# Optimization experiments

Hardware: AMD Instinct MI355X
Metric: run time of the kernel (lower is better)

The kernel has to match this reference:

```python
import jax, jax.numpy as jnp
import numpy as np

NU, NI = 4000, 4000
R, M, OUT = 5, 256, 75
SIDE, FDIM = 64, 128


def setup_inputs() -> dict:
    key = jax.random.key(0)
    ks = jax.random.split(key, 12)
    return {
        "adj_matrix": jax.random.randint(ks[0], (NU, NI), 0, 6, dtype=jnp.int32),
        "u_sideFeat": jax.random.normal(ks[1], (NU, FDIM), dtype=jnp.float32),
        "v_sideFeat": jax.random.normal(ks[2], (NI, FDIM), dtype=jnp.float32),
        "msg_W": jax.random.normal(ks[3], (R, M, NU + NI), dtype=jnp.float32) * 0.05,
        "dense_W": jax.random.normal(ks[4], (OUT, M), dtype=jnp.float32) * 0.05,
        "u_W1": jax.random.normal(ks[5], (SIDE, FDIM), dtype=jnp.float32) * 0.05,
        "u_b1": jax.random.normal(ks[6], (SIDE,), dtype=jnp.float32) * 0.05,
        "u_W2": jax.random.normal(ks[7], (OUT, SIDE), dtype=jnp.float32) * 0.05,
        "v_W1": jax.random.normal(ks[8], (SIDE, FDIM), dtype=jnp.float32) * 0.05,
        "v_b1": jax.random.normal(ks[9], (SIDE,), dtype=jnp.float32) * 0.05,
        "v_W2": jax.random.normal(ks[10], (OUT, SIDE), dtype=jnp.float32) * 0.05,
        "isNegative": 0,
    }


def reference(adj_matrix, u_sideFeat, v_sideFeat, msg_W, dense_W,
              u_W1, u_b1, u_W2, v_W1, v_b1, v_W2, isNegative):
    # isNegative=0, dropout=0 -> one-hot matrices are exact identity slices,
    # so msgLayer(sum_j adj_r[i,j]/C * onehot_j) == (adj_r/C) @ W_r[:, cols].T
    nu, ni = adj_matrix.shape
    r_vals = jnp.arange(1, msg_W.shape[0] + 1, dtype=adj_matrix.dtype)
    # rating-split binary adjacencies [R, NU, NI]
    A = (adj_matrix[None, :, :] == r_vals[:, None, None]).astype(jnp.float32)
    Nu = A.sum(axis=(0, 2))            # user degree over all ratings [NU]
    Nv = A.sum(axis=(0, 1))            # item degree [NI]
    C = jnp.sqrt(Nu[:, None] * Nv[None, :])  # symmetric normalization [NU, NI]
    Csafe = jnp.where(C > 0, C, 1.0)
    An = A / Csafe[None, :, :]
    W_users = msg_W[:, :, :nu]         # [R, M, NU]
    W_items = msg_W[:, :, nu:]         # [R, M, NI]
    # accum='sum' over ratings, then relu
    Hu = jax.nn.relu(jnp.einsum('rui,rmi->um', An, W_items))  # [NU, M]
    Hv = jax.nn.relu(jnp.einsum('rui,rmu->im', An, W_users))  # [NI, M]
    Fu = jax.nn.relu(u_sideFeat @ u_W1.T + u_b1)
    Fv = jax.nn.relu(v_sideFeat @ v_W1.T + v_b1)
    U = jax.nn.relu(Hu @ dense_W.T + Fu @ u_W2.T)
    V = jax.nn.relu(Hv @ dense_W.T + Fv @ v_W2.T)
    return (U, V)
```

## Files before the change

kernel.cpp:

```cpp
#include <hip/hip_runtime.h>
#include <hip/hip_bf16.h>
#include <stdint.h>

#define NU 4000
#define NI 4000
#define RR 5
#define MM 256
#define OUTD 75
#define FDIM 128
#define KP 4096
#define KPH 2048
#define HP_STRIDE 1024000

typedef float f32x4 __attribute__((ext_vector_type(4)));
typedef int   i32x4 __attribute__((ext_vector_type(4)));
typedef short bf16x8 __attribute__((ext_vector_type(8)));

static __device__ __forceinline__ short f2b(float x) {
  __hip_bfloat16 h = __float2bfloat16(x);
  return (short)__builtin_bit_cast(unsigned short, h);
}
static __device__ __forceinline__ float b2f(short x) {
  unsigned int u = ((unsigned int)(unsigned short)x) << 16;
  return __builtin_bit_cast(float, u);
}
static __device__ __forceinline__ bf16x8 cvt8(f32x4 a, f32x4 b) {
  bf16x8 r;
  r[0] = f2b(a[0]); r[1] = f2b(a[1]); r[2] = f2b(a[2]); r[3] = f2b(a[3]);
  r[4] = f2b(b[0]); r[5] = f2b(b[1]); r[6] = f2b(b[2]); r[7] = f2b(b[3]);
  return r;
}

__global__ __launch_bounds__(256) void k_trans(const int* __restrict__ adj,
                                               uint8_t* __restrict__ a8p,
                                               uint8_t* __restrict__ a8tp,
                                               int* __restrict__ Nu,
                                               int* __restrict__ Nv) {
  __shared__ int8_t lp[64][68];
  __shared__ int8_t lt[64][68];
  __shared__ int rowc[64];
  __shared__ int colp[4][64];
  const int i0 = blockIdx.x * 64;
  const int u0 = blockIdx.y * 64;
  const int t = threadIdx.x;
  const int w = t >> 6, lane = t & 63;
  int mycol = 0;
  for (int rep = 0; rep < 16; rep++) {
    const int r = rep * 4 + w;
    const int u = u0 + r, i = i0 + lane;
    int a = (u < NU && i < NI) ? adj[(size_t)u * NI + i] : 0;
    const int nz = (a > 0) ? 1 : 0;
    unsigned long long bal = __ballot(nz);
    if (lane == 0) rowc[r] = (int)__popcll(bal);
    mycol += nz;
    lp[r][lane] = (int8_t)a;
    lt[lane][r] = (int8_t)a;
  }
  colp[w][lane] = mycol;
  __syncthreads();
  {
    const int r = t >> 2, c = t & 3;
    const uint32_t* xp = (const uint32_t*)(&lp[r][c * 16]);
    const uint32_t* xt = (const uint32_t*)(&lt[r][c * 16]);
    uint32_t t0, t1, t2, t3, w0, w1;
    t0 = xp[0] | (xp[0] >> 4); t1 = xp[1] | (xp[1] >> 4);
    t2 = xp[2] | (xp[2] >> 4); t3 = xp[3] | (xp[3] >> 4);
    w0 = __builtin_amdgcn_perm(t1, t0, 0x06040200u);
    w1 = __builtin_amdgcn_perm(t3, t2, 0x06040200u);
    *(uint2*)(a8p + (size_t)(u0 + r) * KPH + (i0 >> 1) + c * 8) = make_uint2(w0, w1);
    t0 = xt[0] | (xt[0] >> 4); t1 = xt[1] | (xt[1] >> 4);
    t2 = xt[2] | (xt[2] >> 4); t3 = xt[3] | (xt[3] >> 4);
    w0 = __builtin_amdgcn_perm(t1, t0, 0x06040200u);
    w1 = __builtin_amdgcn_perm(t3, t2, 0x06040200u);
    *(uint2*)(a8tp + (size_t)(i0 + r) * KPH + (u0 >> 1) + c * 8) = make_uint2(w0, w1);
  }
  if (t < 64) {
    const int cc = colp[0][t] + colp[1][t] + colp[2][t] + colp[3][t];
    if (i0 + t < NI && cc) atomicAdd(&Nv[i0 + t], cc);
    if (u0 + t < NU && rowc[t]) atomicAdd(&Nu[u0 + t], rowc[t]);
  }
}

__global__ __launch_bounds__(256) void k_pbuild(const float* __restrict__ msgW,
                                                const int* __restrict__ Nu,
                                                const int* __restrict__ Nv,
                                                int8_t* __restrict__ Pu,
                                                int8_t* __restrict__ Pv) {
  const int b = blockIdx.x;
  const float* src = msgW + (size_t)b * (NU + NI);
#pragma unroll
  for (int it = 0; it < 2; ++it) {
    const int base = (threadIdx.x + it * 256) * 8;
    uint32_t lou = 0, hiu = 0, lov = 0, hiv = 0;
    if (base < NU) {
      const f32x4 v0 = *(const f32x4*)(src + base);
      const f32x4 v1 = *(const f32x4*)(src + base + 4);
      const f32x4 u0 = *(const f32x4*)(src + NU + base);
      const f32x4 u1 = *(const f32x4*)(src + NU + base + 4);
      const int4 cu0 = *(const int4*)(Nu + base);
      const int4 cu1 = *(const int4*)(Nu + base + 4);
      const int4 cv0 = *(const int4*)(Nv + base);
      const int4 cv1 = *(const int4*)(Nv + base + 4);
      float qv[8], qu[8];
      const int cus[8] = {cu0.x, cu0.y, cu0.z, cu0.w, cu1.x, cu1.y, cu1.z, cu1.w};
      const int cvs[8] = {cv0.x, cv0.y, cv0.z, cv0.w, cv1.x, cv1.y, cv1.z, cv1.w};
      const float vs[8] = {v0[0], v0[1], v0[2], v0[3], v1[0], v1[1], v1[2], v1[3]};
      const float us[8] = {u0[0], u0[1], u0[2], u0[3], u1[0], u1[1], u1[2], u1[3]};
#pragma unroll
      for (int j = 0; j < 8; ++j) {
        const float su = cus[j] > 0 ? rsqrtf((float)cus[j]) * 256.0f : 0.f;
        const float sv = cvs[j] > 0 ? rsqrtf((float)cvs[j]) * 256.0f : 0.f;
        qv[j] = fminf(fmaxf(vs[j] * su, -127.f), 127.f);
        qu[j] = fminf(fmaxf(us[j] * sv, -127.f), 127.f);
      }
      uint32_t bv[8], bu[8];
#pragma unroll
      for (int j = 0; j < 8; ++j) {
        bv[j] = (uint32_t)(uint8_t)(int8_t)__float2int_rn(qv[j]);
        bu[j] = (uint32_t)(uint8_t)(int8_t)__float2int_rn(qu[j]);
      }
      lov = bv[0] | (bv[2] << 8) | (bv[4] << 16) | (bv[6] << 24);
      hiv = bv[1] | (bv[3] << 8) | (bv[5] << 16) | (bv[7] << 24);
      lou = bu[0] | (bu[2] << 8) | (bu[4] << 16) | (bu[6] << 24);
      hiu = bu[1] | (bu[3] << 8) | (bu[5] << 16) | (bu[7] << 24);
    }
    *(uint2*)(Pv + (size_t)b * KP + base) = make_uint2(lov, hiv);
    *(uint2*)(Pu + (size_t)b * KP + base) = make_uint2(lou, hiu);
  }
}

__global__ __launch_bounds__(256) void k_wcvt(const float* __restrict__ dW,
                                              const float* __restrict__ uW1,
                                              const float* __restrict__ vW1,
                                              const float* __restrict__ uW2,
                                              const float* __restrict__ vW2,
                                              __hip_bfloat16* __restrict__ dWb,
                                              __hip_bfloat16* __restrict__ W1b,
                                              __hip_bfloat16* __restrict__ W2b) {
  const int tid = blockIdx.x * 256 + threadIdx.x;
  const int stride = gridDim.x * 256;
  for (int idx = tid; idx < 80 * 256; idx += stride) {
    const int oc = idx >> 8, k = idx & 255;
    dWb[idx] = __float2bfloat16(oc < 75 ? dW[oc * 256 + k] : 0.f);
  }
  for (int idx = tid; idx < 2 * 64 * 128; idx += stride) {
    const int s = idx >> 13, r = idx & 8191;
    W1b[idx] = __float2bfloat16(s ? vW1[r] : uW1[r]);
  }
  for (int idx = tid; idx < 2 * 80 * 64; idx += stride) {
    const int s = idx / 5120, r = idx % 5120;
    const int oc = r >> 6, k = r & 63;
    const float* W2 = s ? vW2 : uW2;
    W2b[idx] = __float2bfloat16(oc < 75 ? W2[oc * 64 + k] : 0.f);
  }
}

#define GLOAD_LDS(g, s) __builtin_amdgcn_global_load_lds( \
    (const __attribute__((address_space(1))) uint32_t*)(g), \
    (__attribute__((address_space(3))) uint32_t*)(s), 16, 0, 0)

static __device__ __forceinline__ uint32_t ohp(uint32_t sel, int r) {
  const uint32_t TL[5] = {0x00000100u, 0x00010000u, 0x01000000u, 0u, 0u};
  const uint32_t TH[5] = {0u, 0u, 0u, 0x00000001u, 0x00000100u};
  return __builtin_amdgcn_perm(TH[r], TL[r], sel);
}

__global__ __launch_bounds__(256, 5) void k_gemm(const uint8_t* __restrict__ Au,
                                                 const uint8_t* __restrict__ Av,
                                                 const int8_t* __restrict__ Pu,
                                                 const int8_t* __restrict__ Pv,
                                                 const int* __restrict__ Nu,
                                                 const int* __restrict__ Nv,
                                                 __hip_bfloat16* __restrict__ Hp) {
  __shared__ __attribute__((aligned(16))) char Bls[2][10240];

  const int bid = blockIdx.x;
  const int side = bid & 1;
  const int bn = (bid >> 1) & 7;
  const int rest = bid >> 4;
  const int ks = rest % 5;
  const int bm = rest / 5;
  const uint8_t* __restrict__ A8 = side ? Av : Au;
  const int8_t* __restrict__ P  = side ? Pv : Pu;
  const int* __restrict__ cnt = side ? Nv : Nu;
  const int kbeg = ks * 832;
  const int nst = (ks == 4) ? 12 : 13;

  const int t = threadIdx.x;
  const int w = t >> 6, l = t & 63;
  const int l15 = l & 15, l4 = l >> 4;

  const int scnt = (w < 2) ? 3 : 2;
  const int nb = (w < 2) ? w * 3 : 6 + (w - 2) * 2;
  uint32_t soff[3], ldst[3];
  {
    const uint32_t jsrc = (uint32_t)((l & 3) ^ ((l >> 3) & 3));
#pragma unroll
    for (int i = 0; i < 3; ++i) {
      const int n = nb + ((i < scnt) ? i : 0);
      const int r = n >> 1, chunk = n & 1;
      const int colg = bn * 32 + chunk * 16 + (l >> 2);
      soff[i] = (uint32_t)(r * 256 + colg) * KP + jsrc * 16u;
      ldst[i] = (uint32_t)(n << 10);
    }
  }
#define STAGE(bi, kk) { \
  GLOAD_LDS(P + soff[0] + (uint32_t)(kk), &Bls[bi][0] + ldst[0]); \
  GLOAD_LDS(P + soff[1] + (uint32_t)(kk), &Bls[bi][0] + ldst[1]); \
  if (scnt == 3) GLOAD_LDS(P + soff[2] + (uint32_t)(kk), &Bls[bi][0] + ldst[2]); }

  const uint32_t rbase = (uint32_t)(l15 * 64) +
                         ((uint32_t)(l4 ^ ((l15 >> 1) & 3)) << 4);

  uint32_t paoff[4];
#pragma unroll
  for (int g = 0; g < 4; ++g)
    paoff[g] = (uint32_t)(bm * 256 + w * 64 + g * 16 + l15) * KPH + l4 * 8;

  i32x4 acc[4][2] = {};
  uint2 aC[4], aN[4];

  STAGE(0, kbeg);
#pragma unroll
  for (int g = 0; g < 4; ++g)
    aC[g] = *(const uint2*)(A8 + paoff[g] + (kbeg >> 1));
  __syncthreads();

  for (int st = 0; st < nst; ++st) {
    const int kk = kbeg + st * 64;
    if (st + 1 < nst) {
      STAGE((st & 1) ^ 1, kk + 64);
#pragma unroll
      for (int g = 0; g < 4; ++g)
        aN[g] = *(const uint2*)(A8 + paoff[g] + ((kk + 64) >> 1));
    }
    uint32_t ud[4][4];
#pragma unroll
    for (int g = 0; g < 4; ++g) {
      ud[g][0] = aC[g].x & 0x0F0F0F0Fu;
      ud[g][1] = (aC[g].x >> 4) & 0x0F0F0F0Fu;
      ud[g][2] = aC[g].y & 0x0F0F0F0Fu;
      ud[g][3] = (aC[g].y >> 4) & 0x0F0F0F0Fu;
    }
    const char* lb = &Bls[st & 1][0];
#pragma unroll
    for (int r = 0; r < 5; ++r) {
      const uint4 B0 = *(const uint4*)(lb + r * 2048 + rbase);
      const uint4 B1 = *(const uint4*)(lb + r * 2048 + rbase + 1024);
#pragma unroll
      for (int g = 0; g < 4; ++g) {
        uint4 af;
        af.x = ohp(ud[g][0], r); af.y = ohp(ud[g][1], r);
        af.z = ohp(ud[g][2], r); af.w = ohp(ud[g][3], r);
        const i32x4 a4 = __builtin_bit_cast(i32x4, af);
        acc[g][0] = __builtin_amdgcn_mfma_i32_16x16x64_i8(
            a4, __builtin_bit_cast(i32x4, B0), acc[g][0], 0, 0, 0);
        acc[g][1] = __builtin_amdgcn_mfma_i32_16x16x64_i8(
            a4, __builtin_bit_cast(i32x4, B1), acc[g][1], 0, 0, 0);
      }
    }
#pragma unroll
    for (int g = 0; g < 4; ++g) aC[g] = aN[g];
    __syncthreads();
  }

  __hip_bfloat16* hp = Hp + (size_t)(ks * 2 + side) * HP_STRIDE;
#pragma unroll
  for (int g = 0; g < 4; ++g) {
    const int rowb = bm * 256 + w * 64 + g * 16 + l4 * 4;
#pragma unroll
    for (int c = 0; c < 2; ++c) {
      const int ocol = bn * 32 + c * 16 + l15;
#pragma unroll
      for (int q = 0; q < 4; ++q) {
        const int orow = rowb + q;
        if (orow < 4000) {
          const int cv = cnt[orow];
          const float s = cv > 0 ? rsqrtf((float)cv) * (1.0f / 256.0f) : 0.f;
          hp[(size_t)orow * 256 + ocol] = __float2bfloat16((float)acc[g][c][q] * s);
        }
      }
    }
  }
#undef STAGE
}

__global__ __launch_bounds__(256) void k_out(const __hip_bfloat16* __restrict__ Hp,
                                             const float* __restrict__ usf,
                                             const float* __restrict__ vsf,
                                             const __hip_bfloat16* __restrict__ dWb,
                                             const __hip_bfloat16* __restrict__ W1b,
                                             const float* __restrict__ ub1,
                                             const float* __restrict__ vb1,
                                             const __hip_bfloat16* __restrict__ W2b,
                                             float* __restrict__ out) {
  const int bid = blockIdx.x;
  const int side = bid / 125, rb = bid % 125;
  const int t = threadIdx.x, w = t >> 6, l = t & 63;
  const int rowg = w >> 1, kh = w & 1;
  const int l15 = l & 15, l4 = l >> 4;
  const float* __restrict__ sf = side ? vsf : usf;
  const float* __restrict__ b1 = side ? vb1 : ub1;
  const __hip_bfloat16* __restrict__ W1 = W1b + side * (64 * 128);
  const __hip_bfloat16* __restrict__ W2 = W2b + side * (80 * 64);
  const __hip_bfloat16* __restrict__ hp = Hp + (size_t)side * HP_STRIDE;
  const int r0 = rb * 32 + rowg * 16;
  const int myrow = r0 + l15;

  __shared__ __hip_bfloat16 lf[2][16][72];
  __shared__ float ps[2][80][20];

  f32x4 oA[5] = {};
  const __hip_bfloat16* hbase = hp + (size_t)myrow * 256 + 8 * l4;

#define PHASE_B_HALF(kb) { \
  _Pragma("unroll") \
  for (int i_ = 0; i_ < 4; ++i_) { \
    const int kk_ = (kb) + i_ * 32; \
    const bf16x8 q0 = *(const bf16x8*)(hbase + kk_); \
    const bf16x8 q1 = *(const bf16x8*)(hbase + 2 * HP_STRIDE + kk_); \
    const bf16x8 q2 = *(const bf16x8*)(hbase + 4 * HP_STRIDE + kk_); \
    const bf16x8 q3 = *(const bf16x8*)(hbase + 6 * HP_STRIDE + kk_); \
    const bf16x8 q4 = *(const bf16x8*)(hbase + 8 * HP_STRIDE + kk_); \
    bf16x8 af; \
    _Pragma("unroll") \
    for (int j_ = 0; j_ < 8; ++j_) { \
      float hv = b2f(q0[j_]) + b2f(q1[j_]) + b2f(q2[j_]) + b2f(q3[j_]) + b2f(q4[j_]); \
      af[j_] = f2b(hv > 0.f ? hv : 0.f); \
    } \
    _Pragma("unroll") \
    for (int c_ = 0; c_ < 5; ++c_) { \
      const bf16x8 bf = *(const bf16x8*)(dWb + (c_ * 16 + l15) * 256 + kk_ + 8 * l4); \
      oA[c_] = __builtin_amdgcn_mfma_f32_16x16x32_bf16(af, bf, oA[c_], 0, 0, 0); \
    } \
  } }

  if (kh == 0) {
    f32x4 fA[4] = {};
#pragma unroll
    for (int kk = 0; kk < 128; kk += 32) {
      const float* psf = sf + (size_t)myrow * 128 + kk + 8 * l4;
      const bf16x8 af = cvt8(*(const f32x4*)psf, *(const f32x4*)(psf + 4));
#pragma unroll
      for (int c = 0; c < 4; ++c) {
        const bf16x8 bf = *(const bf16x8*)(W1 + (c * 16 + l15) * 128 + kk + 8 * l4);
        fA[c] = __builtin_amdgcn_mfma_f32_16x16x32_bf16(af, bf, fA[c], 0, 0, 0);
      }
    }
#pragma unroll
    for (int c = 0; c < 4; ++c) {
      const float bv = b1[c * 16 + l15];
#pragma unroll
      for (int reg = 0; reg < 4; ++reg) {
        float v = fA[c][reg] + bv;
        lf[rowg][l4 * 4 + reg][c * 16 + l15] = __float2bfloat16(v > 0.f ? v : 0.f);
      }
    }
  } else {
    PHASE_B_HALF(128)
  }
  __syncthreads();
  if (kh == 0) {
    PHASE_B_HALF(0)
  } else {
#pragma unroll
    for (int kk = 0; kk < 64; kk += 32) {
      const bf16x8 af = *(const bf16x8*)(&lf[rowg][l15][kk + 8 * l4]);
#pragma unroll
      for (int c = 0; c < 5; ++c) {
        const bf16x8 bf = *(const bf16x8*)(W2 + (c * 16 + l15) * 64 + kk + 8 * l4);
        oA[c] = __builtin_amdgcn_mfma_f32_16x16x32_bf16(af, bf, oA[c], 0, 0, 0);
      }
    }
#pragma unroll
    for (int c = 0; c < 5; ++c)
      *(f32x4*)&ps[rowg][c * 16 + l15][l4 * 4] = oA[c];
  }
  __syncthreads();
  if (kh == 0) {
    float* po = out + (size_t)side * (4000 * 75);
#pragma unroll
    for (int c = 0; c < 5; ++c) {
      const int oc = c * 16 + l15;
      if (oc < 75) {
        const f32x4 pv = *(const f32x4*)&ps[rowg][oc][l4 * 4];
#pragma unroll
        for (int reg = 0; reg < 4; ++reg) {
          const int orow = r0 + l4 * 4 + reg;
          const float v = oA[c][reg] + pv[reg];
          po[(size_t)orow * 75 + oc] = v > 0.f ? v : 0.f;
        }
      }
    }
  }
#undef PHASE_B_HALF
}

extern "C" void kernel_launch(void* const* d_in, const int* in_sizes, int n_in,
                              void* d_out, int out_size, void* d_ws, size_t ws_size,
                              hipStream_t stream) {
  const int* adj = (const int*)d_in[0];
  const float* usf = (const float*)d_in[1];
  const float* vsf = (const float*)d_in[2];
  const float* msgW = (const float*)d_in[3];
  const float* dW = (const float*)d_in[4];
  const float* uW1 = (const float*)d_in[5];
  const float* ub1 = (const float*)d_in[6];
  const float* uW2 = (const float*)d_in[7];
  const float* vW1 = (const float*)d_in[8];
  const float* vb1 = (const float*)d_in[9];
  const float* vW2 = (const float*)d_in[10];
  float* out = (float*)d_out;

  char* w = (char*)d_ws;
  const size_t A_BYTES = (size_t)4096 * KPH;
  const size_t P_BYTES = (size_t)RR * MM * KP;
  const size_t HP_BYTES = (size_t)10 * HP_STRIDE * 2;
  int* Nu = (int*)w;
  int* Nv = (int*)(w + 16384);
  uint8_t* Au = (uint8_t*)(w + 32768);
  uint8_t* Av = Au + A_BYTES;
  int8_t* Pu = (int8_t*)(w + 32768 + 2 * A_BYTES);
  int8_t* Pv = Pu + P_BYTES;
  __hip_bfloat16* Hp = (__hip_bfloat16*)(w + 32768 + 2 * A_BYTES + 2 * P_BYTES);
  char* wb = (char*)(Hp) + HP_BYTES;
  __hip_bfloat16* dWb = (__hip_bfloat16*)wb;
  __hip_bfloat16* W1b = (__hip_bfloat16*)(wb + 40960);
  __hip_bfloat16* W2b = (__hip_bfloat16*)(wb + 40960 + 32768);
  const size_t need = 32768 + 2 * A_BYTES + 2 * P_BYTES + HP_BYTES + 94208;
  if (ws_size < need) return;

  hipMemsetAsync(w, 0, 32768, stream);
  k_wcvt<<<64, 256, 0, stream>>>(dW, uW1, vW1, uW2, vW2, dWb, W1b, W2b);
  k_trans<<<dim3(64, 64), 256, 0, stream>>>(adj, Au, Av, Nu, Nv);
  k_pbuild<<<1280, 256, 0, stream>>>(msgW, Nu, Nv, Pu, Pv);
  k_gemm<<<1280, 256, 0, stream>>>(Au, Av, Pu, Pv, Nu, Nv, Hp);
  k_out<<<250, 256, 0, stream>>>(Hp, usf, vsf, dWb, W1b, ub1, vb1, W2b, out);
}
```

Before: 102.0 us.

## Widen GEMM N-tile to 64, use six K-splits, fold weight conversion into pbuild

The int8 GEMM now gives each block 64 output columns instead of 32, which doubles accumulator registers and LDS staging per block. This lets each A fragment feed four MFMAs instead of two. The K range is split six ways instead of five, so 768 blocks replace 1280, and k_out sums six partial Hp buffers. The separate weight-conversion kernel becomes an extra block in k_pbuild, saving one launch. In exchange, occupancy drops (launch bounds go from 5 to 3) and the partial-sum buffer grows.

Result: slower. 135.3 us (+32.7%).

```diff
diff --git a/kernel.cpp b/kernel.cpp
--- a/kernel.cpp
+++ b/kernel.cpp
@@ -85,8 +85,34 @@
                                                 const int* __restrict__ Nu,
                                                 const int* __restrict__ Nv,
                                                 int8_t* __restrict__ Pu,
-                                                int8_t* __restrict__ Pv) {
+                                                int8_t* __restrict__ Pv,
+                                                const float* __restrict__ dW,
+                                                const float* __restrict__ uW1,
+                                                const float* __restrict__ vW1,
+                                                const float* __restrict__ uW2,
+                                                const float* __restrict__ vW2,
+                                                __hip_bfloat16* __restrict__ dWb,
+                                                __hip_bfloat16* __restrict__ W1b,
+                                                __hip_bfloat16* __restrict__ W2b) {
   const int b = blockIdx.x;
+  if (b == 1280) {
+    const int tid = threadIdx.x;
+    for (int idx = tid; idx < 80 * 256; idx += 256) {
+      const int oc = idx >> 8, k = idx & 255;
+      dWb[idx] = __float2bfloat16(oc < 75 ? dW[oc * 256 + k] : 0.f);
+    }
+    for (int idx = tid; idx < 2 * 64 * 128; idx += 256) {
+      const int s = idx >> 13, r = idx & 8191;
+      W1b[idx] = __float2bfloat16(s ? vW1[r] : uW1[r]);
+    }
+    for (int idx = tid; idx < 2 * 80 * 64; idx += 256) {
+      const int s = idx / 5120, r = idx % 5120;
+      const int oc = r >> 6, k = r & 63;
+      const float* W2 = s ? vW2 : uW2;
+      W2b[idx] = __float2bfloat16(oc < 75 ? W2[oc * 64 + k] : 0.f);
+    }
+    return;
+  }
   const float* src = msgW + (size_t)b * (NU + NI);
 #pragma unroll
   for (int it = 0; it < 2; ++it) {
@@ -129,32 +155,6 @@
   }
 }
 
-__global__ __launch_bounds__(256) void k_wcvt(const float* __restrict__ dW,
-                                              const float* __restrict__ uW1,
-                                              const float* __restrict__ vW1,
-                                              const float* __restrict__ uW2,
-                                              const float* __restrict__ vW2,
-                                              __hip_bfloat16* __restrict__ dWb,
-                                              __hip_bfloat16* __restrict__ W1b,
-                                              __hip_bfloat16* __restrict__ W2b) {
-  const int tid = blockIdx.x * 256 + threadIdx.x;
-  const int stride = gridDim.x * 256;
-  for (int idx = tid; idx < 80 * 256; idx += stride) {
-    const int oc = idx >> 8, k = idx & 255;
-    dWb[idx] = __float2bfloat16(oc < 75 ? dW[oc * 256 + k] : 0.f);
-  }
-  for (int idx = tid; idx < 2 * 64 * 128; idx += stride) {
-    const int s = idx >> 13, r = idx & 8191;
-    W1b[idx] = __float2bfloat16(s ? vW1[r] : uW1[r]);
-  }
-  for (int idx = tid; idx < 2 * 80 * 64; idx += stride) {
-    const int s = idx / 5120, r = idx % 5120;
-    const int oc = r >> 6, k = r & 63;
-    const float* W2 = s ? vW2 : uW2;
-    W2b[idx] = __float2bfloat16(oc < 75 ? W2[oc * 64 + k] : 0.f);
-  }
-}
-
 #define GLOAD_LDS(g, s) __builtin_amdgcn_global_load_lds( \
     (const __attribute__((address_space(1))) uint32_t*)(g), \
     (__attribute__((address_space(3))) uint32_t*)(s), 16, 0, 0)
@@ -165,49 +165,46 @@
   return __builtin_amdgcn_perm(TH[r], TL[r], sel);
 }
 
-__global__ __launch_bounds__(256, 5) void k_gemm(const uint8_t* __restrict__ Au,
+__global__ __launch_bounds__(256, 3) void k_gemm(const uint8_t* __restrict__ Au,
                                                  const uint8_t* __restrict__ Av,
                                                  const int8_t* __restrict__ Pu,
                                                  const int8_t* __restrict__ Pv,
                                                  const int* __restrict__ Nu,
                                                  const int* __restrict__ Nv,
                                                  __hip_bfloat16* __restrict__ Hp) {
-  __shared__ __attribute__((aligned(16))) char Bls[2][10240];
+  __shared__ __attribute__((aligned(16))) char Bls[2][20480];
 
   const int bid = blockIdx.x;
   const int side = bid & 1;
-  const int bn = (bid >> 1) & 7;
-  const int rest = bid >> 4;
-  const int ks = rest % 5;
-  const int bm = rest / 5;
+  const int bn = (bid >> 1) & 3;
+  const int rest = bid >> 3;
+  const int ks = rest % 6;
+  const int bm = rest / 6;
   const uint8_t* __restrict__ A8 = side ? Av : Au;
   const int8_t* __restrict__ P  = side ? Pv : Pu;
   const int* __restrict__ cnt = side ? Nv : Nu;
-  const int kbeg = ks * 832;
-  const int nst = (ks == 4) ? 12 : 13;
+  const int kbeg = (ks < 4) ? ks * 704 : 2816 + (ks - 4) * 640;
+  const int nst = (ks < 4) ? 11 : 10;
 
   const int t = threadIdx.x;
   const int w = t >> 6, l = t & 63;
   const int l15 = l & 15, l4 = l >> 4;
 
-  const int scnt = (w < 2) ? 3 : 2;
-  const int nb = (w < 2) ? w * 3 : 6 + (w - 2) * 2;
-  uint32_t soff[3], ldst[3];
+  uint32_t soff[5], ldst[5];
   {
     const uint32_t jsrc = (uint32_t)((l & 3) ^ ((l >> 3) & 3));
 #pragma unroll
-    for (int i = 0; i < 3; ++i) {
-      const int n = nb + ((i < scnt) ? i : 0);
-      const int r = n >> 1, chunk = n & 1;
-      const int colg = bn * 32 + chunk * 16 + (l >> 2);
+    for (int i = 0; i < 5; ++i) {
+      const int n = w * 5 + i;
+      const int r = n >> 2, chunk = n & 3;
+      const int colg = bn * 64 + chunk * 16 + (l >> 2);
       soff[i] = (uint32_t)(r * 256 + colg) * KP + jsrc * 16u;
       ldst[i] = (uint32_t)(n << 10);
     }
   }
-#define STAGE(bi, kk) { \
-  GLOAD_LDS(P + soff[0] + (uint32_t)(kk), &Bls[bi][0] + ldst[0]); \
-  GLOAD_LDS(P + soff[1] + (uint32_t)(kk), &Bls[bi][0] + ldst[1]); \
-  if (scnt == 3) GLOAD_LDS(P + soff[2] + (uint32_t)(kk), &Bls[bi][0] + ldst[2]); }
+#define STAGE(bi, kk) { _Pragma("unroll") \
+  for (int i_ = 0; i_ < 5; ++i_) \
+    GLOAD_LDS(P + soff[i_] + (uint32_t)(kk), &Bls[bi][0] + ldst[i_]); }
 
   const uint32_t rbase = (uint32_t)(l15 * 64) +
                          ((uint32_t)(l4 ^ ((l15 >> 1) & 3)) << 4);
@@ -217,7 +214,7 @@
   for (int g = 0; g < 4; ++g)
     paoff[g] = (uint32_t)(bm * 256 + w * 64 + g * 16 + l15) * KPH + l4 * 8;
 
-  i32x4 acc[4][2] = {};
+  i32x4 acc[4][4] = {};
   uint2 aC[4], aN[4];
 
   STAGE(0, kbeg);
@@ -245,8 +242,10 @@
     const char* lb = &Bls[st & 1][0];
 #pragma unroll
     for (int r = 0; r < 5; ++r) {
-      const uint4 B0 = *(const uint4*)(lb + r * 2048 + rbase);
-      const uint4 B1 = *(const uint4*)(lb + r * 2048 + rbase + 1024);
+      const uint4 B0 = *(const uint4*)(lb + r * 4096 + rbase);
+      const uint4 B1 = *(const uint4*)(lb + r * 4096 + rbase + 1024);
+      const uint4 B2 = *(const uint4*)(lb + r * 4096 + rbase + 2048);
+      const uint4 B3 = *(const uint4*)(lb + r * 4096 + rbase + 3072);
 #pragma unroll
       for (int g = 0; g < 4; ++g) {
         uint4 af;
@@ -257,6 +256,10 @@
             a4, __builtin_bit_cast(i32x4, B0), acc[g][0], 0, 0, 0);
         acc[g][1] = __builtin_amdgcn_mfma_i32_16x16x64_i8(
             a4, __builtin_bit_cast(i32x4, B1), acc[g][1], 0, 0, 0);
+        acc[g][2] = __builtin_amdgcn_mfma_i32_16x16x64_i8(
+            a4, __builtin_bit_cast(i32x4, B2), acc[g][2], 0, 0, 0);
+        acc[g][3] = __builtin_amdgcn_mfma_i32_16x16x64_i8(
+            a4, __builtin_bit_cast(i32x4, B3), acc[g][3], 0, 0, 0);
       }
     }
 #pragma unroll
@@ -269,8 +272,8 @@
   for (int g = 0; g < 4; ++g) {
     const int rowb = bm * 256 + w * 64 + g * 16 + l4 * 4;
 #pragma unroll
-    for (int c = 0; c < 2; ++c) {
-      const int ocol = bn * 32 + c * 16 + l15;
+    for (int c = 0; c < 4; ++c) {
+      const int ocol = bn * 64 + c * 16 + l15;
 #pragma unroll
       for (int q = 0; q < 4; ++q) {
         const int orow = rowb + q;
@@ -322,10 +325,12 @@
     const bf16x8 q2 = *(const bf16x8*)(hbase + 4 * HP_STRIDE + kk_); \
     const bf16x8 q3 = *(const bf16x8*)(hbase + 6 * HP_STRIDE + kk_); \
     const bf16x8 q4 = *(const bf16x8*)(hbase + 8 * HP_STRIDE + kk_); \
+    const bf16x8 q5 = *(const bf16x8*)(hbase + 10 * HP_STRIDE + kk_); \
     bf16x8 af; \
     _Pragma("unroll") \
     for (int j_ = 0; j_ < 8; ++j_) { \
-      float hv = b2f(q0[j_]) + b2f(q1[j_]) + b2f(q2[j_]) + b2f(q3[j_]) + b2f(q4[j_]); \
+      float hv = b2f(q0[j_]) + b2f(q1[j_]) + b2f(q2[j_]) + b2f(q3[j_]) + \
+                 b2f(q4[j_]) + b2f(q5[j_]); \
       af[j_] = f2b(hv > 0.f ? hv : 0.f); \
     } \
     _Pragma("unroll") \
@@ -415,7 +420,7 @@
   char* w = (char*)d_ws;
   const size_t A_BYTES = (size_t)4096 * KPH;
   const size_t P_BYTES = (size_t)RR * MM * KP;
-  const size_t HP_BYTES = (size_t)10 * HP_STRIDE * 2;
+  const size_t HP_BYTES = (size_t)12 * HP_STRIDE * 2;
   int* Nu = (int*)w;
   int* Nv = (int*)(w + 16384);
   uint8_t* Au = (uint8_t*)(w + 32768);
@@ -431,9 +436,9 @@
   if (ws_size < need) return;
 
   hipMemsetAsync(w, 0, 32768, stream);
-  k_wcvt<<<64, 256, 0, stream>>>(dW, uW1, vW1, uW2, vW2, dWb, W1b, W2b);
   k_trans<<<dim3(64, 64), 256, 0, stream>>>(adj, Au, Av, Nu, Nv);
-  k_pbuild<<<1280, 256, 0, stream>>>(msgW, Nu, Nv, Pu, Pv);
-  k_gemm<<<1280, 256, 0, stream>>>(Au, Av, Pu, Pv, Nu, Nv, Hp);
+  k_pbuild<<<1281, 256, 0, stream>>>(msgW, Nu, Nv, Pu, Pv, dW, uW1, vW1, uW2,
+                                     vW2, dWb, W1b, W2b);
+  k_gemm<<<768, 256, 0, stream>>>(Au, Av, Pu, Pv, Nu, Nv, Hp);
   k_out<<<250, 256, 0, stream>>>(Hp, usf, vsf, dWb, W1b, ub1, vb1, W2b, out);
 }
```
